# Optimization experiments

Hardware: AMD Instinct MI355X
Metric: run time of the kernel (lower is better)

Reference implementation:

```python
import jax, jax.numpy as jnp
import numpy as np
from jax import lax

B, C, L, K = 8, 256, 4096, 65
PAD = K // 2  # torch: int(kernel.shape[-1] / 2) = 32 -> same-length output for odd K


def depthwise_corr(x, k):
    """Depthwise cross-correlation (torch conv1d semantics, no kernel flip).
    x: [B, C, L] float32, k: [K] float32 (same kernel shared by all channels,
    matching kernel.repeat(seq_len, 1)). Returns [B, C, L]."""
    w = jnp.broadcast_to(k.reshape(1, 1, K), (C, 1, K))  # [C, 1, K]
    return lax.conv_general_dilated(
        x, w, window_strides=(1,), padding=[(PAD, PAD)],
        dimension_numbers=("NCH", "OIH", "NCH"), feature_group_count=C)


def setup_inputs() -> dict:
    key = jax.random.key(0)
    k1, k2, k3 = jax.random.split(key, 3)
    return {
        "x": jax.random.normal(k1, (B, C, L), dtype=jnp.float32),
        "kernel_real": jax.random.normal(k2, (K,), dtype=jnp.float32),
        "kernel_imag": jax.random.normal(k3, (K,), dtype=jnp.float32),
        "weights_mag": jnp.ones((1, C, 1), dtype=jnp.float32),
        "weights_angle": jnp.ones((1, C, 1), dtype=jnp.float32),
    }


def reference(x, kernel_real, kernel_imag, weights_mag, weights_angle):
    # mf_coeffs = conj(kernel) -> weight = kernel_real - 1j*kernel_imag.
    # Input x is real (imag=0 after .to(complex64)), so complex conv splits
    # into two real depthwise correlations.
    yr = depthwise_corr(x, kernel_real)            # [B, C, L]
    yi = -depthwise_corr(x, kernel_imag)           # [B, C, L]
    y = lax.complex(yr, yi)                        # complex64 [B, C, L]

    # torch.std over dims (1,2), unbiased (correction=1), complex -> real std
    mean = jnp.mean(y, axis=(1, 2), keepdims=True)
    n = C * L
    var = jnp.sum(jnp.abs(y - mean) ** 2, axis=(1, 2), keepdims=True) / (n - 1)
    y = y / jnp.sqrt(var)                          # real std broadcasts over complex

    # weights_mag * y * exp(-1j * weights_angle)
    phase = lax.complex(jnp.cos(weights_angle), -jnp.sin(weights_angle))  # [1, C, 1]
    y = weights_mag * y * phase

    # FFT over the channel dim (dim=-2), then fftshift on that dim
    return jnp.fft.fftshift(jnp.fft.fft(y, axis=-2), axes=-2)
```

## Files before the change

kernel.cpp:

```cpp
#include <hip/hip_runtime.h>
#include <math.h>

#define NB 8
#define NC 256
#define NL 4096
#define NK 65
#define NSL (NL / 16)

typedef float vf4 __attribute__((ext_vector_type(4)));
typedef float vf2 __attribute__((ext_vector_type(2)));

__device__ float4 g_part[NB * NSL];

__device__ __forceinline__ int lidx(int row, int q) {
    return (row << 3) + (q ^ (row & 7));
}

#define LOAD16(W, off)                                                      \
    {                                                                       \
        const int g0_ = l0 + (off);                                         \
        if (g0_ >= 0 && g0_ + 16 <= NL) {         \
            _Pragma("unroll")                                               \
            for (int q = 0; q < 4; ++q) {                                   \
                const float4 v_ = *(const float4*)(xr + g0_ + 4 * q);       \
                W[4*q+0] = v_.x; W[4*q+1] = v_.y;                           \
                W[4*q+2] = v_.z; W[4*q+3] = v_.w;                           \
            }                                                               \
        } else {                                                            \
            _Pragma("unroll")                                               \
            for (int q = 0; q < 16; ++q) {                                  \
                const int g_ = g0_ + q;                                     \
                W[q] = (g_ >= 0 && g_ < NL) ? xr[g_] : 0.0f;                \
            }                                                               \
        }                                                                   \
    }

#define CHUNK16(Lo, Hi, tb)                                                 \
    {                                                                       \
        _Pragma("unroll")                                                   \
        for (int j2 = 0; j2 < 16; ++j2) {                                   \
            const float kr_ = kre[(tb) + j2];        \
            const float ki_ = kim[(tb) + j2];                               \
            _Pragma("unroll")                                               \
            for (int i = 0; i < 16; ++i) {                                  \
                const int wi_ = i + j2;                                     \
                const float xv_ = (wi_ < 16) ? Lo[wi_] : Hi[wi_ - 16];      \
                sr[i] = fmaf(xv_, kr_, sr[i]);                              \
                si[i] = fmaf(xv_, ki_, si[i]);                              \
            }                                                               \
        }                                                                   \
    }

__device__ __forceinline__ int digitrev_shift(int pp) {
    int k = ((pp & 3) << 6) | (((pp >> 2) & 3) << 4)
          | (((pp >> 4) & 3) << 2) | ((pp >> 6) & 3);
    return k ^ 128;
}

__global__ __launch_bounds__(256, 4) void fused_conv_fft_kernel(
    const float* __restrict__ x,
    const float* __restrict__ kre,
    const float* __restrict__ kim,
    const float* __restrict__ wmag,
    const float* __restrict__ wang,
    float* __restrict__ out,
    int out_size)
{
    __shared__ __align__(16) float4 lbuf4[NC * 9];

    const int t = threadIdx.x;
    const int b = blockIdx.x & 7;
    const int st = blockIdx.x >> 3;
    const int l0 = st << 4;
    const int lane = t & 63, wv = t >> 6;

    const float* xr = x + (size_t)b * NC * NL + (size_t)t * NL;
    const bool interleaved = (out_size >= 2 * NB * NC * NL);

    float sr[16], si[16];
    #pragma unroll
    for (int i = 0; i < 16; ++i) { sr[i] = 0.0f; si[i] = 0.0f; }

    float W0[16], W1[16], W2[16], W3[16];
    LOAD16(W0, -32);
    LOAD16(W1, -16);
    LOAD16(W2, 0);
    LOAD16(W3, 16);
    CHUNK16(W0, W1, 0);
    LOAD16(W0, 32);
    CHUNK16(W1, W2, 16);
    CHUNK16(W2, W3, 32);
    CHUNK16(W3, W0, 48);
    {
        const float kr_ = kre[64];
        const float ki_ = kim[64];
        #pragma unroll
        for (int i = 0; i < 16; ++i) {
            sr[i] = fmaf(W0[i], kr_, sr[i]);
            si[i] = fmaf(W0[i], ki_, si[i]);
        }
    }

    float tsr = 0.0f, tsi = 0.0f, tsq = 0.0f;
    #pragma unroll
    for (int i = 0; i < 16; ++i) {
        tsr += sr[i];
        tsi -= si[i];
        tsq = fmaf(sr[i], sr[i], tsq);
        tsq = fmaf(si[i], si[i], tsq);
    }

    float sw, cw;
    sincosf(wang[t], &sw, &cw);
    const float wm = wmag[t];
    const float wgr =  wm * cw;
    const float wgi = -wm * sw;
    float tw64r, tw64i;
    {
        float ang = (float)lane * 0.024543692606170260f;
        float s, c;
        sincosf(ang, &s, &c);
        tw64r = c; tw64i = -s;
    }

    #pragma unroll
    for (int k = 0; k < 8; ++k) {
        float4 o;
        o.x = sr[2*k]   * wgr + si[2*k]   * wgi;
        o.y = sr[2*k]   * wgi - si[2*k]   * wgr;
        o.z = sr[2*k+1] * wgr + si[2*k+1] * wgi;
        o.w = sr[2*k+1] * wgi - si[2*k+1] * wgr;
        lbuf4[lidx(t, k)] = o;
    }
    __syncthreads();

    #pragma unroll
    for (int s = 0; s < 4; ++s) {
        const int shift = 2 * s;
        const int q = 64 >> shift;
        #pragma unroll
        for (int it = 0; it < 2; ++it) {
            int task = it * 256 + t;
            int lpp = task & 7;
            int m = task >> 3;
            int j = m & (q - 1);
            int blk = m >> (6 - shift);
            int base2 = blk << (8 - shift);

            int ca = base2 + j;
            float4 a0 = lbuf4[lidx(ca, lpp)];
            float4 a1 = lbuf4[lidx(ca + q, lpp)];
            float4 a2 = lbuf4[lidx(ca + 2*q, lpp)];
            float4 a3 = lbuf4[lidx(ca + 3*q, lpp)];

            float w1r, w1i;
            if (s < 3) {
                int e = j << shift;
                w1r = __shfl(tw64r, e);
                w1i = __shfl(tw64i, e);
            } else {
                w1r = 1.0f; w1i = 0.0f;
            }
            float w2r = fmaf(w1r, w1r, -(w1i * w1i));
            float w2i = 2.0f * w1r * w1i;
            float w3r = w2r * w1r - w2i * w1i;
            float w3i = w2r * w1i + w2i * w1r;

            float4 b0, b1, b2, b3;
            {
                float t0r = a0.x + a2.x, t0i = a0.y + a2.y;
                float t1r = a0.x - a2.x, t1i = a0.y - a2.y;
                float t2r = a1.x + a3.x, t2i = a1.y + a3.y;
                float t3r = a1.x - a3.x, t3i = a1.y - a3.y;
                b0.x = t0r + t2r;       b0.y = t0i + t2i;
                float b2r = t0r - t2r,  b2i = t0i - t2i;
                float b1r = t1r + t3i,  b1i = t1i - t3r;
                float b3r = t1r - t3i,  b3i = t1i + t3r;
                b1.x = b1r*w1r - b1i*w1i;  b1.y = b1r*w1i + b1i*w1r;
                b2.x = b2r*w2r - b2i*w2i;  b2.y = b2r*w2i + b2i*w2r;
                b3.x = b3r*w3r - b3i*w3i;  b3.y = b3r*w3i + b3i*w3r;
            }
            {
                float t0r = a0.z + a2.z, t0i = a0.w + a2.w;
                float t1r = a0.z - a2.z, t1i = a0.w - a2.w;
                float t2r = a1.z + a3.z, t2i = a1.w + a3.w;
                float t3r = a1.z - a3.z, t3i = a1.w - a3.w;
                b0.z = t0r + t2r;       b0.w = t0i + t2i;
                float b2r = t0r - t2r,  b2i = t0i - t2i;
                float b1r = t1r + t3i,  b1i = t1i - t3r;
                float b3r = t1r - t3i,  b3i = t1i + t3r;
                b1.z = b1r*w1r - b1i*w1i;  b1.w = b1r*w1i + b1i*w1r;
                b2.z = b2r*w2r - b2i*w2i;  b2.w = b2r*w2i + b2i*w2r;
                b3.z = b3r*w3r - b3i*w3i;  b3.w = b3r*w3i + b3i*w3r;
            }
            lbuf4[lidx(ca, lpp)]         = b0;
            lbuf4[lidx(ca + q, lpp)]     = b1;
            lbuf4[lidx(ca + 2*q, lpp)]   = b2;
            lbuf4[lidx(ca + 3*q, lpp)]   = b3;
        }
        __syncthreads();
    }

    #pragma unroll
    for (int it = 0; it < 8; ++it) {
        int task = it * 256 + t;
        int lpp = task & 7;
        int pp = task >> 3;
        float4 v = lbuf4[lidx(pp, lpp)];
        int cout = digitrev_shift(pp);
        if (interleaved) {
            size_t fi = 2 * ((size_t)(b * NC + cout) * NL + l0) + 4 * lpp;
            if (fi + 4 <= (size_t)out_size) {
                vf4 o4; o4.x = v.x; o4.y = v.y; o4.z = v.z; o4.w = v.w;
                __builtin_nontemporal_store(o4, (vf4*)(out + fi));
            }
        } else {
            size_t fi = (size_t)(b * NC + cout) * NL + l0 + 2 * lpp;
            if (fi + 2 <= (size_t)out_size) {
                vf2 o2; o2.x = v.x; o2.y = v.z;
                __builtin_nontemporal_store(o2, (vf2*)(out + fi));
            }
        }
    }

    #pragma unroll
    for (int off = 32; off > 0; off >>= 1) {
        tsr += __shfl_down(tsr, off);
        tsi += __shfl_down(tsi, off);
        tsq += __shfl_down(tsq, off);
    }
    __syncthreads();
    float* redf = (float*)lbuf4;
    if (lane == 0) { redf[wv*3+0] = tsr; redf[wv*3+1] = tsi; redf[wv*3+2] = tsq; }
    __syncthreads();
    if (t == 0) {
        float a0 = 0.0f, a1 = 0.0f, a2 = 0.0f;
        #pragma unroll
        for (int i = 0; i < 4; ++i) { a0 += redf[i*3]; a1 += redf[i*3+1]; a2 += redf[i*3+2]; }
        g_part[b * NSL + st] = make_float4(a0, a1, a2, 0.0f);
    }
}

__global__ __launch_bounds__(256) void scale_out_kernel(
    float* __restrict__ out, int out_size)
{
    __shared__ float sred[13];
    const int t = threadIdx.x;
    const int j = blockIdx.x;
    const int b = j & 7;
    const int seg = j >> 3;
    const int lane = t & 63, wv = t >> 6;

    float4 p = g_part[b * NSL + t];
    float psr = p.x, psi = p.y, psq = p.z;
    #pragma unroll
    for (int off = 32; off > 0; off >>= 1) {
        psr += __shfl_down(psr, off);
        psi += __shfl_down(psi, off);
        psq += __shfl_down(psq, off);
    }
    if (lane == 0) { sred[wv*3+0] = psr; sred[wv*3+1] = psi; sred[wv*3+2] = psq; }
    __syncthreads();
    if (t == 0) {
        float a0 = 0.0f, a1 = 0.0f, a2 = 0.0f;
        #pragma unroll
        for (int i = 0; i < 4; ++i) { a0 += sred[i*3]; a1 += sred[i*3+1]; a2 += sred[i*3+2]; }
        const float n = (float)(NC * NL);
        float var = (a2 - (a0*a0 + a1*a1)/n) / (n - 1.0f);
        sred[12] = rsqrtf(var);
    }
    __syncthreads();
    const float inv = sred[12];

    const int fpbatch = out_size >> 3;
    const int fpseg = fpbatch >> 8;
    const int base = b * fpbatch + seg * fpseg;
    if ((fpseg & 3) == 0 && ((size_t)(out + base) & 15) == 0) {
        const int n4 = fpseg >> 2;
        for (int i = t; i < n4; i += 256) {
            vf4* p4 = (vf4*)(out + base) + i;
            vf4 v = __builtin_nontemporal_load(p4);
            v.x *= inv; v.y *= inv; v.z *= inv; v.w *= inv;
            __builtin_nontemporal_store(v, p4);
        }
    } else {
        for (int i = t; i < fpseg; i += 256) out[base + i] *= inv;
    }
    if (j == 2047) {
        for (int i = ((out_size >> 11) << 11) + t; i < out_size; i += 256)
            out[i] *= inv;
    }
}

extern "C" void kernel_launch(void* const* d_in, const int* in_sizes, int n_in,
                              void* d_out, int out_size, void* d_ws, size_t ws_size,
                              hipStream_t stream)
{
    const float* x   = (const float*)d_in[0];
    const float* kre = (const float*)d_in[1];
    const float* kim = (const float*)d_in[2];
    const float* wm  = (const float*)d_in[3];
    const float* wa  = (const float*)d_in[4];
    float* out = (float*)d_out;
    (void)d_ws; (void)ws_size;

    fused_conv_fft_kernel<<<NB * NSL, 256, 0, stream>>>(x, kre, kim, wm, wa,
                                                        out, out_size);
    scale_out_kernel<<<2048, 256, 0, stream>>>(out, out_size);
}
```

Before: 141.7 us.

## Process two L-tiles per block and prefetch second tile loads during FFT

Each block now handles two consecutive 16-wide sequence tiles instead of one, halving the grid to 1024 blocks. Global loads for the second tile are issued before and during the first tile's shared-memory FFT and store, so memory latency can overlap compute. The partial-statistics array shrinks to 128 entries per batch, and the reduction kernel masks the unused threads. This raises register pressure from the extra prefetch buffers and halves block count, which may reduce occupancy or parallelism.

```diff
diff --git a/kernel.cpp b/kernel.cpp
--- a/kernel.cpp
+++ b/kernel.cpp
@@ -5,20 +5,20 @@
 #define NC 256
 #define NL 4096
 #define NK 65
-#define NSL (NL / 16)
+#define NSP 128
 
 typedef float vf4 __attribute__((ext_vector_type(4)));
 typedef float vf2 __attribute__((ext_vector_type(2)));
 
-__device__ float4 g_part[NB * NSL];
+__device__ float4 g_part[NB * NSP];
 
 __device__ __forceinline__ int lidx(int row, int q) {
     return (row << 3) + (q ^ (row & 7));
 }
 
-#define LOAD16(W, off)                                                      \
+#define LOAD16(W, L0, off)                                                  \
     {                                                                       \
-        const int g0_ = l0 + (off);                                         \
+        const int g0_ = (L0) + (off);                                       \
         if (g0_ >= 0 && g0_ + 16 <= NL) {         \
             _Pragma("unroll")                                               \
             for (int q = 0; q < 4; ++q) {                                   \
@@ -51,11 +51,128 @@
         }                                                                   \
     }
 
+#define TAIL64(W)                                                           \
+    {                                                                       \
+        const float kr_ = kre[64];                                          \
+        const float ki_ = kim[64];                                          \
+        _Pragma("unroll")                                                   \
+        for (int i = 0; i < 16; ++i) {                                      \
+            sr[i] = fmaf(W[i], kr_, sr[i]);                                 \
+            si[i] = fmaf(W[i], ki_, si[i]);                                 \
+        }                                                                   \
+    }
+
+#define STATS_AND_WEIGHT()                                                  \
+    {                                                                       \
+        _Pragma("unroll")                                                   \
+        for (int i = 0; i < 16; ++i) {                                      \
+            tsr += sr[i];                                                   \
+            tsi -= si[i];                                                   \
+            tsq = fmaf(sr[i], sr[i], tsq);                                  \
+            tsq = fmaf(si[i], si[i], tsq);                                  \
+        }                                                                   \
+        _Pragma("unroll")                                                   \
+        for (int k = 0; k < 8; ++k) {                                       \
+            float4 o;                                                       \
+            o.x = sr[2*k]   * wgr + si[2*k]   * wgi;                        \
+            o.y = sr[2*k]   * wgi - si[2*k]   * wgr;                        \
+            o.z = sr[2*k+1] * wgr + si[2*k+1] * wgi;                        \
+            o.w = sr[2*k+1] * wgi - si[2*k+1] * wgr;                        \
+            lbuf4[lidx(t, k)] = o;                                          \
+        }                                                                   \
+    }
+
 __device__ __forceinline__ int digitrev_shift(int pp) {
     int k = ((pp & 3) << 6) | (((pp >> 2) & 3) << 4)
           | (((pp >> 4) & 3) << 2) | ((pp >> 6) & 3);
     return k ^ 128;
 }
+
+#define FFT256()                                                            \
+    _Pragma("unroll")                                                       \
+    for (int s = 0; s < 4; ++s) {                                           \
+        const int shift = 2 * s;                                            \
+        const int q = 64 >> shift;                                          \
+        _Pragma("unroll")                                                   \
+        for (int it = 0; it < 2; ++it) {                                    \
+            int task = it * 256 + t;                                        \
+            int lpp = task & 7;                                             \
+            int m = task >> 3;                                              \
+            int j = m & (q - 1);                                            \
+            int blk = m >> (6 - shift);                                     \
+            int base2 = blk << (8 - shift);                                 \
+            int ca = base2 + j;                                             \
+            float4 a0 = lbuf4[lidx(ca, lpp)];                               \
+            float4 a1 = lbuf4[lidx(ca + q, lpp)];                           \
+            float4 a2 = lbuf4[lidx(ca + 2*q, lpp)];                         \
+            float4 a3 = lbuf4[lidx(ca + 3*q, lpp)];                         \
+            float w1r, w1i;                                                 \
+            if (s < 3) {                                                    \
+                int e = j << shift;                                         \
+                w1r = __shfl(tw64r, e);                                     \
+                w1i = __shfl(tw64i, e);                                     \
+            } else { w1r = 1.0f; w1i = 0.0f; }                              \
+            float w2r = fmaf(w1r, w1r, -(w1i * w1i));                      \
+            float w2i = 2.0f * w1r * w1i;                                   \
+            float w3r = w2r * w1r - w2i * w1i;                              \
+            float w3i = w2r * w1i + w2i * w1r;                              \
+            float4 b0, b1, b2, b3;                                          \
+            {                                                               \
+                float t0r = a0.x + a2.x, t0i = a0.y + a2.y;                 \
+                float t1r = a0.x - a2.x, t1i = a0.y - a2.y;                 \
+                float t2r = a1.x + a3.x, t2i = a1.y + a3.y;                 \
+                float t3r = a1.x - a3.x, t3i = a1.y - a3.y;                 \
+                b0.x = t0r + t2r;       b0.y = t0i + t2i;                   \
+                float b2r = t0r - t2r,  b2i = t0i - t2i;                    \
+                float b1r = t1r + t3i,  b1i = t1i - t3r;                    \
+                float b3r = t1r - t3i,  b3i = t1i + t3r;                    \
+                b1.x = b1r*w1r - b1i*w1i;  b1.y = b1r*w1i + b1i*w1r;        \
+                b2.x = b2r*w2r - b2i*w2i;  b2.y = b2r*w2i + b2i*w2r;        \
+                b3.x = b3r*w3r - b3i*w3i;  b3.y = b3r*w3i + b3i*w3r;        \
+            }                                                               \
+            {                                                               \
+                float t0r = a0.z + a2.z, t0i = a0.w + a2.w;                 \
+                float t1r = a0.z - a2.z, t1i = a0.w - a2.w;                 \
+                float t2r = a1.z + a3.z, t2i = a1.w + a3.w;                 \
+                float t3r = a1.z - a3.z, t3i = a1.w - a3.w;                 \
+                b0.z = t0r + t2r;       b0.w = t0i + t2i;                   \
+                float b2r = t0r - t2r,  b2i = t0i - t2i;                    \
+                float b1r = t1r + t3i,  b1i = t1i - t3r;                    \
+                float b3r = t1r - t3i,  b3i = t1i + t3r;                    \
+                b1.z = b1r*w1r - b1i*w1i;  b1.w = b1r*w1i + b1i*w1r;        \
+                b2.z = b2r*w2r - b2i*w2i;  b2.w = b2r*w2i + b2i*w2r;        \
+                b3.z = b3r*w3r - b3i*w3i;  b3.w = b3r*w3i + b3i*w3r;        \
+            }                                                               \
+            lbuf4[lidx(ca, lpp)]         = b0;                              \
+            lbuf4[lidx(ca + q, lpp)]     = b1;                              \
+            lbuf4[lidx(ca + 2*q, lpp)]   = b2;                              \
+            lbuf4[lidx(ca + 3*q, lpp)]   = b3;                              \
+        }                                                                   \
+        __syncthreads();                                                    \
+    }
+
+#define STORE_TILE(L0)                                                      \
+    _Pragma("unroll")                                                       \
+    for (int it = 0; it < 8; ++it) {                                        \
+        int task = it * 256 + t;                                            \
+        int lpp = task & 7;                                                 \
+        int pp = task >> 3;                                                 \
+        float4 v = lbuf4[lidx(pp, lpp)];                                    \
+        int cout = digitrev_shift(pp);                                      \
+        if (interleaved) {                                                  \
+            size_t fi = 2 * ((size_t)(b * NC + cout) * NL + (L0)) + 4 * lpp;\
+            if (fi + 4 <= (size_t)out_size) {                               \
+                vf4 o4; o4.x = v.x; o4.y = v.y; o4.z = v.z; o4.w = v.w;     \
+                __builtin_nontemporal_store(o4, (vf4*)(out + fi));          \
+            }                                                               \
+        } else {                                                            \
+            size_t fi = (size_t)(b * NC + cout) * NL + (L0) + 2 * lpp;      \
+            if (fi + 2 <= (size_t)out_size) {                               \
+                vf2 o2; o2.x = v.x; o2.y = v.z;                             \
+                __builtin_nontemporal_store(o2, (vf2*)(out + fi));          \
+            }                                                               \
+        }                                                                   \
+    }
 
 __global__ __launch_bounds__(256, 4) void fused_conv_fft_kernel(
     const float* __restrict__ x,
@@ -70,45 +187,30 @@
 
     const int t = threadIdx.x;
     const int b = blockIdx.x & 7;
-    const int st = blockIdx.x >> 3;
-    const int l0 = st << 4;
+    const int sp = blockIdx.x >> 3;
+    const int l0A = sp << 5;
+    const int l0B = l0A + 16;
     const int lane = t & 63, wv = t >> 6;
 
     const float* xr = x + (size_t)b * NC * NL + (size_t)t * NL;
     const bool interleaved = (out_size >= 2 * NB * NC * NL);
 
+    float tsr = 0.0f, tsi = 0.0f, tsq = 0.0f;
     float sr[16], si[16];
+
     #pragma unroll
     for (int i = 0; i < 16; ++i) { sr[i] = 0.0f; si[i] = 0.0f; }
-
     float W0[16], W1[16], W2[16], W3[16];
-    LOAD16(W0, -32);
-    LOAD16(W1, -16);
-    LOAD16(W2, 0);
-    LOAD16(W3, 16);
+    LOAD16(W0, l0A, -32);
+    LOAD16(W1, l0A, -16);
+    LOAD16(W2, l0A, 0);
+    LOAD16(W3, l0A, 16);
     CHUNK16(W0, W1, 0);
-    LOAD16(W0, 32);
+    LOAD16(W0, l0A, 32);
     CHUNK16(W1, W2, 16);
     CHUNK16(W2, W3, 32);
     CHUNK16(W3, W0, 48);
-    {
-        const float kr_ = kre[64];
-        const float ki_ = kim[64];
-        #pragma unroll
-        for (int i = 0; i < 16; ++i) {
-            sr[i] = fmaf(W0[i], kr_, sr[i]);
-            si[i] = fmaf(W0[i], ki_, si[i]);
-        }
-    }
-
-    float tsr = 0.0f, tsi = 0.0f, tsq = 0.0f;
-    #pragma unroll
-    for (int i = 0; i < 16; ++i) {
-        tsr += sr[i];
-        tsi -= si[i];
-        tsq = fmaf(sr[i], sr[i], tsq);
-        tsq = fmaf(si[i], si[i], tsq);
-    }
+    TAIL64(W0);
 
     float sw, cw;
     sincosf(wang[t], &sw, &cw);
@@ -123,105 +225,38 @@
         tw64r = c; tw64i = -s;
     }
 
+    STATS_AND_WEIGHT();
+
+    float B0[16], B1[16];
+    LOAD16(B0, l0B, -32);
+    LOAD16(B1, l0B, -16);
+
+    __syncthreads();
+    FFT256();
+
+    float B2[16], B3[16];
+    LOAD16(B2, l0B, 0);
+    LOAD16(B3, l0B, 16);
+
+    STORE_TILE(l0A);
+
     #pragma unroll
-    for (int k = 0; k < 8; ++k) {
-        float4 o;
-        o.x = sr[2*k]   * wgr + si[2*k]   * wgi;
-        o.y = sr[2*k]   * wgi - si[2*k]   * wgr;
-        o.z = sr[2*k+1] * wgr + si[2*k+1] * wgi;
-        o.w = sr[2*k+1] * wgi - si[2*k+1] * wgr;
-        lbuf4[lidx(t, k)] = o;
-    }
-    __syncthreads();
-
-    #pragma unroll
-    for (int s = 0; s < 4; ++s) {
-        const int shift = 2 * s;
-        const int q = 64 >> shift;
-        #pragma unroll
-        for (int it = 0; it < 2; ++it) {
-            int task = it * 256 + t;
-            int lpp = task & 7;
-            int m = task >> 3;
-            int j = m & (q - 1);
-            int blk = m >> (6 - shift);
-            int base2 = blk << (8 - shift);
-
-            int ca = base2 + j;
-            float4 a0 = lbuf4[lidx(ca, lpp)];
-            float4 a1 = lbuf4[lidx(ca + q, lpp)];
-            float4 a2 = lbuf4[lidx(ca + 2*q, lpp)];
-            float4 a3 = lbuf4[lidx(ca + 3*q, lpp)];
-
-            float w1r, w1i;
-            if (s < 3) {
-                int e = j << shift;
-                w1r = __shfl(tw64r, e);
-                w1i = __shfl(tw64i, e);
-            } else {
-                w1r = 1.0f; w1i = 0.0f;
-            }
-            float w2r = fmaf(w1r, w1r, -(w1i * w1i));
-            float w2i = 2.0f * w1r * w1i;
-            float w3r = w2r * w1r - w2i * w1i;
-            float w3i = w2r * w1i + w2i * w1r;
-
-            float4 b0, b1, b2, b3;
-            {
-                float t0r = a0.x + a2.x, t0i = a0.y + a2.y;
-                float t1r = a0.x - a2.x, t1i = a0.y - a2.y;
-                float t2r = a1.x + a3.x, t2i = a1.y + a3.y;
-                float t3r = a1.x - a3.x, t3i = a1.y - a3.y;
-                b0.x = t0r + t2r;       b0.y = t0i + t2i;
-                float b2r = t0r - t2r,  b2i = t0i - t2i;
-                float b1r = t1r + t3i,  b1i = t1i - t3r;
-                float b3r = t1r - t3i,  b3i = t1i + t3r;
-                b1.x = b1r*w1r - b1i*w1i;  b1.y = b1r*w1i + b1i*w1r;
-                b2.x = b2r*w2r - b2i*w2i;  b2.y = b2r*w2i + b2i*w2r;
-                b3.x = b3r*w3r - b3i*w3i;  b3.y = b3r*w3i + b3i*w3r;
-            }
-            {
-                float t0r = a0.z + a2.z, t0i = a0.w + a2.w;
-                float t1r = a0.z - a2.z, t1i = a0.w - a2.w;
-                float t2r = a1.z + a3.z, t2i = a1.w + a3.w;
-                float t3r = a1.z - a3.z, t3i = a1.w - a3.w;
-                b0.z = t0r + t2r;       b0.w = t0i + t2i;
-                float b2r = t0r - t2r,  b2i = t0i - t2i;
-                float b1r = t1r + t3i,  b1i = t1i - t3r;
-                float b3r = t1r - t3i,  b3i = t1i + t3r;
-                b1.z = b1r*w1r - b1i*w1i;  b1.w = b1r*w1i + b1i*w1r;
-                b2.z = b2r*w2r - b2i*w2i;  b2.w = b2r*w2i + b2i*w2r;
-                b3.z = b3r*w3r - b3i*w3i;  b3.w = b3r*w3i + b3i*w3r;
-            }
-            lbuf4[lidx(ca, lpp)]         = b0;
-            lbuf4[lidx(ca + q, lpp)]     = b1;
-            lbuf4[lidx(ca + 2*q, lpp)]   = b2;
-            lbuf4[lidx(ca + 3*q, lpp)]   = b3;
-        }
-        __syncthreads();
-    }
-
-    #pragma unroll
-    for (int it = 0; it < 8; ++it) {
-        int task = it * 256 + t;
-        int lpp = task & 7;
-        int pp = task >> 3;
-        float4 v = lbuf4[lidx(pp, lpp)];
-        int cout = digitrev_shift(pp);
-        if (interleaved) {
-            size_t fi = 2 * ((size_t)(b * NC + cout) * NL + l0) + 4 * lpp;
-            if (fi + 4 <= (size_t)out_size) {
-                vf4 o4; o4.x = v.x; o4.y = v.y; o4.z = v.z; o4.w = v.w;
-                __builtin_nontemporal_store(o4, (vf4*)(out + fi));
-            }
-        } else {
-            size_t fi = (size_t)(b * NC + cout) * NL + l0 + 2 * lpp;
-            if (fi + 2 <= (size_t)out_size) {
-                vf2 o2; o2.x = v.x; o2.y = v.z;
-                __builtin_nontemporal_store(o2, (vf2*)(out + fi));
-            }
-        }
-    }
+    for (int i = 0; i < 16; ++i) { sr[i] = 0.0f; si[i] = 0.0f; }
+    LOAD16(W0, l0B, 32);
+    CHUNK16(B0, B1, 0);
+    CHUNK16(B1, B2, 16);
+    CHUNK16(B2, B3, 32);
+    CHUNK16(B3, W0, 48);
+    TAIL64(W0);
+
+    __syncthreads();
+
+    STATS_AND_WEIGHT();
+
+    __syncthreads();
+    FFT256();
+
+    STORE_TILE(l0B);
 
     #pragma unroll
     for (int off = 32; off > 0; off >>= 1) {
@@ -237,7 +272,7 @@
         float a0 = 0.0f, a1 = 0.0f, a2 = 0.0f;
         #pragma unroll
         for (int i = 0; i < 4; ++i) { a0 += redf[i*3]; a1 += redf[i*3+1]; a2 += redf[i*3+2]; }
-        g_part[b * NSL + st] = make_float4(a0, a1, a2, 0.0f);
+        g_part[b * NSP + sp] = make_float4(a0, a1, a2, 0.0f);
     }
 }
 
@@ -251,8 +286,11 @@
     const int seg = j >> 3;
     const int lane = t & 63, wv = t >> 6;
 
-    float4 p = g_part[b * NSL + t];
-    float psr = p.x, psi = p.y, psq = p.z;
+    float psr = 0.0f, psi = 0.0f, psq = 0.0f;
+    if (t < NSP) {
+        float4 p = g_part[b * NSP + t];
+        psr = p.x; psi = p.y; psq = p.z;
+    }
     #pragma unroll
     for (int off = 32; off > 0; off >>= 1) {
         psr += __shfl_down(psr, off);
@@ -304,7 +342,7 @@
     float* out = (float*)d_out;
     (void)d_ws; (void)ws_size;
 
-    fused_conv_fft_kernel<<<NB * NSL, 256, 0, stream>>>(x, kre, kim, wm, wa,
+    fused_conv_fft_kernel<<<NB * NSP, 256, 0, stream>>>(x, kre, kim, wm, wa,
                                                         out, out_size);
     scale_out_kernel<<<2048, 256, 0, stream>>>(out, out_size);
 }
```

After: 171.2 us. 20.9% more time.
